# Kernel optimization log

Measured on AMD Instinct MI355X. Metric: run time of the kernel, lower is better.

The kernel has to match this reference:

```python
import jax, jax.numpy as jnp
import numpy as np


def _bilinear_crop(feat, grid):
    """Bilinear sampling with border clamping (BilinearSamplerBHWD semantics).

    feat: [R, C, H, W] float features (one feature map per RoI)
    grid: [R, gh, gw, 2] normalized coords in [-1, 1], channel order (y, x)
    returns: [R, C, gh, gw]
    """
    R, C, H, W = feat.shape
    # unnormalize: -1 -> 0, +1 -> H-1 / W-1
    y = (grid[..., 0] + 1.0) * (H - 1) * 0.5   # [R, gh, gw]
    x = (grid[..., 1] + 1.0) * (W - 1) * 0.5

    y0 = jnp.floor(y)
    x0 = jnp.floor(x)
    wy = y - y0  # fractional parts
    wx = x - x0

    y0i = jnp.clip(y0.astype(jnp.int32), 0, H - 1)
    y1i = jnp.clip(y0.astype(jnp.int32) + 1, 0, H - 1)
    x0i = jnp.clip(x0.astype(jnp.int32), 0, W - 1)
    x1i = jnp.clip(x0.astype(jnp.int32) + 1, 0, W - 1)

    r = jnp.arange(R)[:, None, None]  # [R,1,1] broadcast over grid
    # advanced indexing -> [R, gh, gw, C]
    v00 = feat[r, :, y0i, x0i]
    v01 = feat[r, :, y0i, x1i]
    v10 = feat[r, :, y1i, x0i]
    v11 = feat[r, :, y1i, x1i]

    wy = wy[..., None]
    wx = wx[..., None]
    out = (v00 * (1 - wy) * (1 - wx) + v01 * (1 - wy) * wx
           + v10 * wy * (1 - wx) + v11 * wy * wx)  # [R, gh, gw, C]
    return jnp.transpose(out, (0, 3, 1, 2))  # [R, C, gh, gw]


def setup_inputs() -> dict:
    key = jax.random.key(0)
    k1, k2 = jax.random.split(key)
    R, C, H, W = 128, 512, 37, 37
    GS = 14  # pool_size * 2 (crop_resize_with_max_pool=True)
    input1 = jax.random.normal(k1, (R, C, H, W), dtype=jnp.float32)
    # normalized sampling grid in [-1, 1], channel order (y, x)
    input2 = jax.random.uniform(k2, (R, GS, GS, 2), dtype=jnp.float32,
                                minval=-1.0, maxval=1.0)
    return {"input1": input1, "input2": input2}


def reference(input1, input2):
    return _bilinear_crop(input1, input2)
```

## Files before the change

### kernel.cpp

```cpp
#include <hip/hip_runtime.h>
#include <hip/hip_bf16.h>


#define RR 128
#define CC 512
#define HH 37
#define WW 37
#define GS 14
#define NP (GS * GS)
#define PLANE (HH * WW)
#define CPB 4
#define NBLK (RR * (CC / CPB))

__global__ __launch_bounds__(256) void roicrop_kernel(
    const float* __restrict__ feat,
    const float* __restrict__ grid,
    float* __restrict__ out)
{
    __shared__ float s_plane[CPB * PLANE];
    __shared__ float s_wy[NP];
    __shared__ float s_wx[NP];
    __shared__ int   s_o00[NP];
    __shared__ int   s_o01[NP];
    __shared__ int   s_o10[NP];
    __shared__ int   s_o11[NP];

    const int blk = blockIdx.x;
    const int r  = blk / (CC / CPB);
    const int cb = blk % (CC / CPB);
    const int c0 = cb * CPB;
    const int tid = threadIdx.x;

    if (tid < NP) {
        const int p = tid;
        float gy = grid[((size_t)r * NP + p) * 2 + 0];
        float gx = grid[((size_t)r * NP + p) * 2 + 1];
        float y = (gy + 1.0f) * ((HH - 1) * 0.5f);
        float x = (gx + 1.0f) * ((WW - 1) * 0.5f);
        float y0f = floorf(y);
        float x0f = floorf(x);
        s_wy[p] = y - y0f;
        s_wx[p] = x - x0f;
        int y0 = (int)y0f;
        int x0 = (int)x0f;
        int y0i = min(max(y0,     0), HH - 1);
        int y1i = min(max(y0 + 1, 0), HH - 1);
        int x0i = min(max(x0,     0), WW - 1);
        int x1i = min(max(x0 + 1, 0), WW - 1);
        s_o00[p] = y0i * WW + x0i;
        s_o01[p] = y0i * WW + x1i;
        s_o10[p] = y1i * WW + x0i;
        s_o11[p] = y1i * WW + x1i;
    }

    const float* src = feat + ((size_t)r * CC + c0) * PLANE;
    const float4* src4 = reinterpret_cast<const float4*>(src);
    float4* s4 = reinterpret_cast<float4*>(s_plane);
    #pragma unroll
    for (int i = tid; i < (CPB * PLANE) / 4; i += 256) {
        s4[i] = src4[i];
    }

    __syncthreads();

    float* dst = out + ((size_t)r * CC + c0) * NP;
    #pragma unroll
    for (int o = tid; o < CPB * NP; o += 256) {
        const int cl = o / NP;
        const int p  = o - cl * NP;
        const float wy = s_wy[p];
        const float wx = s_wx[p];
        const float* pl = s_plane + cl * PLANE;
        float v00 = pl[s_o00[p]];
        float v01 = pl[s_o01[p]];
        float v10 = pl[s_o10[p]];
        float v11 = pl[s_o11[p]];
        float top = v00 + (v01 - v00) * wx;
        float bot = v10 + (v11 - v10) * wx;
        dst[o] = top + (bot - top) * wy;
    }
}

extern "C" void kernel_launch(void* const* d_in, const int* in_sizes, int n_in,
                              void* d_out, int out_size, void* d_ws, size_t ws_size,
                              hipStream_t stream) {
    const float* feat = (const float*)d_in[0];
    const float* grid = (const float*)d_in[1];
    float* out = (float*)d_out;
    roicrop_kernel<<<dim3(NBLK), dim3(256), 0, stream>>>(feat, grid, out);
}
```

Baseline: 82.04 us.

## Stream feature planes directly into LDS and vectorize output stores

Replaces the register-staged float4 copy of the feature planes with direct global-to-LDS loads, issued before the per-point coordinate setup so the two overlap. Per-point weights and packed 16-bit offsets now sit in a single float4 LDS table. Each of 196 threads computes four consecutive outputs and writes them as one float4 store. The risk is that the copy loop skips any trailing chunk shorter than 16 bytes, and only 196 of 256 threads do the interpolation.

```diff
diff --git a/kernel.cpp b/kernel.cpp
--- a/kernel.cpp
+++ b/kernel.cpp
@@ -1,5 +1,6 @@
 #include <hip/hip_runtime.h>
 #include <hip/hip_bf16.h>
+#include <stdint.h>
 
 
 #define RR 128
@@ -11,73 +12,81 @@
 #define PLANE (HH * WW)
 #define CPB 4
 #define NBLK (RR * (CC / CPB))
+#define PLANE_BYTES (CPB * PLANE * 4)
+#define NCHUNK ((PLANE_BYTES + 1023) / 1024)
+
+typedef __attribute__((address_space(1))) const void gconst_void;
+typedef __attribute__((address_space(3))) void lds_void;
 
 __global__ __launch_bounds__(256) void roicrop_kernel(
     const float* __restrict__ feat,
     const float* __restrict__ grid,
     float* __restrict__ out)
 {
-    __shared__ float s_plane[CPB * PLANE];
-    __shared__ float s_wy[NP];
-    __shared__ float s_wx[NP];
-    __shared__ int   s_o00[NP];
-    __shared__ int   s_o01[NP];
-    __shared__ int   s_o10[NP];
-    __shared__ int   s_o11[NP];
+    __shared__ float  s_plane[CPB * PLANE];
+    __shared__ float4 s_pt[NP];
 
     const int blk = blockIdx.x;
-    const int r  = blk / (CC / CPB);
-    const int cb = blk % (CC / CPB);
-    const int c0 = cb * CPB;
-    const int tid = threadIdx.x;
+    const int r   = blk / (CC / CPB);
+    const int cb  = blk % (CC / CPB);
+    const int c0  = cb * CPB;
+    const int tid  = threadIdx.x;
+    const int wave = tid >> 6;
+    const int lane = tid & 63;
+
+    const char* src = (const char*)(feat + ((size_t)r * CC + c0) * PLANE);
+    char* lds_base = (char*)s_plane;
+    #pragma unroll
+    for (int ch = wave; ch < NCHUNK; ch += 4) {
+        const int off = ch * 1024 + lane * 16;
+        if (off + 16 <= PLANE_BYTES) {
+            __builtin_amdgcn_global_load_lds(
+                (gconst_void*)(src + off),
+                (lds_void*)(lds_base + ch * 1024 + lane * 16),
+                16, 0, 0);
+        }
+    }
 
     if (tid < NP) {
-        const int p = tid;
-        float gy = grid[((size_t)r * NP + p) * 2 + 0];
-        float gx = grid[((size_t)r * NP + p) * 2 + 1];
-        float y = (gy + 1.0f) * ((HH - 1) * 0.5f);
-        float x = (gx + 1.0f) * ((WW - 1) * 0.5f);
-        float y0f = floorf(y);
-        float x0f = floorf(x);
-        s_wy[p] = y - y0f;
-        s_wx[p] = x - x0f;
-        int y0 = (int)y0f;
-        int x0 = (int)x0f;
+        float2 g2 = reinterpret_cast<const float2*>(grid)[(size_t)r * NP + tid];
+        float y = (g2.x + 1.0f) * 18.0f;
+        float x = (g2.y + 1.0f) * 18.0f;
+        float y0f = floorf(y), x0f = floorf(x);
+        float wy = y - y0f, wx = x - x0f;
+        int y0 = (int)y0f, x0 = (int)x0f;
         int y0i = min(max(y0,     0), HH - 1);
         int y1i = min(max(y0 + 1, 0), HH - 1);
         int x0i = min(max(x0,     0), WW - 1);
         int x1i = min(max(x0 + 1, 0), WW - 1);
-        s_o00[p] = y0i * WW + x0i;
-        s_o01[p] = y0i * WW + x1i;
-        s_o10[p] = y1i * WW + x0i;
-        s_o11[p] = y1i * WW + x1i;
-    }
-
-    const float* src = feat + ((size_t)r * CC + c0) * PLANE;
-    const float4* src4 = reinterpret_cast<const float4*>(src);
-    float4* s4 = reinterpret_cast<float4*>(s_plane);
-    #pragma unroll
-    for (int i = tid; i < (CPB * PLANE) / 4; i += 256) {
-        s4[i] = src4[i];
+        uint32_t oa = (uint32_t)(y0i * WW + x0i) | ((uint32_t)(y0i * WW + x1i) << 16);
+        uint32_t ob = (uint32_t)(y1i * WW + x0i) | ((uint32_t)(y1i * WW + x1i) << 16);
+        s_pt[tid] = make_float4(wy, wx, __uint_as_float(oa), __uint_as_float(ob));
     }
 
     __syncthreads();
 
-    float* dst = out + ((size_t)r * CC + c0) * NP;
-    #pragma unroll
-    for (int o = tid; o < CPB * NP; o += 256) {
-        const int cl = o / NP;
-        const int p  = o - cl * NP;
-        const float wy = s_wy[p];
-        const float wx = s_wx[p];
+    if (tid < NP) {
+        const int cl = tid / 49;
+        const int j  = tid - cl * 49;
+        const int p0 = j * 4;
         const float* pl = s_plane + cl * PLANE;
-        float v00 = pl[s_o00[p]];
-        float v01 = pl[s_o01[p]];
-        float v10 = pl[s_o10[p]];
-        float v11 = pl[s_o11[p]];
-        float top = v00 + (v01 - v00) * wx;
-        float bot = v10 + (v11 - v10) * wx;
-        dst[o] = top + (bot - top) * wy;
+        float4 o;
+        float* op = &o.x;
+        #pragma unroll
+        for (int k = 0; k < 4; ++k) {
+            float4 pt = s_pt[p0 + k];
+            uint32_t oa = __float_as_uint(pt.z);
+            uint32_t ob = __float_as_uint(pt.w);
+            float v00 = pl[oa & 0xffffu];
+            float v01 = pl[oa >> 16];
+            float v10 = pl[ob & 0xffffu];
+            float v11 = pl[ob >> 16];
+            float top = v00 + (v01 - v00) * pt.y;
+            float bot = v10 + (v11 - v10) * pt.y;
+            op[k] = top + (bot - top) * pt.x;
+        }
+        float4* dst = reinterpret_cast<float4*>(out + ((size_t)r * CC + c0) * NP);
+        dst[tid] = o;
     }
 }
 
```

Result: no change. 80.78 us (-1.5%).
